# Kernel optimization log

Hardware: AMD Instinct MI355X
Metric: run time of the kernel (lower is better)

## Reference

```python
import jax, jax.numpy as jnp
import numpy as np

B, S, D_IN, D_OUT, H = 2, 2048, 1024, 1024, 16
HD = D_OUT // H


def setup_inputs() -> dict:
    key = jax.random.key(0)
    ks = jax.random.split(key, 7)
    sc = 0.02
    return {
        "x": jax.random.normal(ks[0], (B, S, D_IN), jnp.float32),
        "attention_mask": jnp.ones((B, S), dtype=bool),
        "W_query": jax.random.normal(ks[1], (D_IN, D_OUT), jnp.float32) * sc,
        "W_key": jax.random.normal(ks[2], (D_IN, D_OUT), jnp.float32) * sc,
        "W_value": jax.random.normal(ks[3], (D_IN, D_OUT), jnp.float32) * sc,
        "W_out": jax.random.normal(ks[4], (D_OUT, D_OUT), jnp.float32) * sc,
        "b_out": jnp.zeros((D_OUT,), jnp.float32),
    }


def reference(x, attention_mask, W_query, W_key, W_value, W_out, b_out):
    b, n, _ = x.shape
    # projections -> (b, H, n, hd)
    def split_heads(t):
        return t.reshape(b, n, H, HD).transpose(0, 2, 1, 3)
    q = split_heads(x @ W_query)
    k = split_heads(x @ W_key)
    v = split_heads(x @ W_value)
    scores = jnp.einsum("bhqd,bhkd->bhqk", q, k)  # (b,H,n,n)
    neg_inf = jnp.float32(-jnp.inf)
    causal = jnp.triu(jnp.ones((n, n), dtype=bool), k=1)  # True above diagonal
    scores = jnp.where(causal[None, None], neg_inf, scores)
    pad = attention_mask[:, None, None, :]  # (b,1,1,n)
    scores = jnp.where(~pad, neg_inf, scores)
    attn = jax.nn.softmax(scores / jnp.float32(np.sqrt(HD)), axis=-1)
    ctx = jnp.einsum("bhqk,bhkd->bhqd", attn, v)
    ctx = ctx.transpose(0, 2, 1, 3).reshape(b, n, D_OUT)
    return ctx @ W_out + b_out
```

## Files before the change

### kernel.cpp

```cpp
#include <hip/hip_runtime.h>
#include <hip/hip_bf16.h>

typedef __bf16 bf16;
typedef __bf16 bf16x4 __attribute__((ext_vector_type(4)));
typedef __bf16 bf16x8 __attribute__((ext_vector_type(8)));
typedef float  f32x4  __attribute__((ext_vector_type(4)));

#define B_    2
#define S_    2048
#define DIN   1024
#define DOUT  1024
#define H_    16
#define HD    64
#define M_TOT (B_ * S_)

__device__ __forceinline__ void gload16(const void* g, void* l) {
  __builtin_amdgcn_global_load_lds(
      (__attribute__((address_space(1))) void*)(g),
      (__attribute__((address_space(3))) void*)(l), 16, 0, 0);
}

__global__ __launch_bounds__(256) void cast_x_k(const float* __restrict__ x,
                                                bf16* __restrict__ xb, int n4) {
  int i = blockIdx.x * 256 + threadIdx.x;
  if (i < n4) {
    float4 v = ((const float4*)x)[i];
    bf16x4 o = {(bf16)v.x, (bf16)v.y, (bf16)v.z, (bf16)v.w};
    ((bf16x4*)xb)[i] = o;
  }
}

__global__ __launch_bounds__(256) void transpose_cast_k(
    const float* __restrict__ wq, const float* __restrict__ wk,
    const float* __restrict__ wv, const float* __restrict__ wo,
    bf16* __restrict__ wqkv_t, bf16* __restrict__ wot) {
  __shared__ float tile[32][33];
  const int z = blockIdx.z;
  const float* src = (z == 0) ? wq : (z == 1) ? wk : (z == 2) ? wv : wo;
  bf16* dst = (z < 3) ? (wqkv_t + (size_t)z * DOUT * DIN) : wot;
  const int bx = blockIdx.x * 32;
  const int by = blockIdx.y * 32;
  const int tx = threadIdx.x & 31, ty = threadIdx.x >> 5;
#pragma unroll
  for (int i = 0; i < 32; i += 8)
    tile[ty + i][tx] = src[(size_t)(by + ty + i) * DOUT + bx + tx];
  __syncthreads();
#pragma unroll
  for (int i = 0; i < 32; i += 8)
    dst[(size_t)(bx + ty + i) * DIN + by + tx] = (bf16)tile[tx][ty + i];
}

template <int MODE>
__global__ __launch_bounds__(256, 2) void gemm_k(
    const bf16* __restrict__ A, const bf16* __restrict__ Bt,
    bf16* __restrict__ Qb, bf16* __restrict__ Kb, bf16* __restrict__ Vt,
    float* __restrict__ Out, const float* __restrict__ bias, int N, int K) {
  __shared__ bf16 Als[128 * 64];
  __shared__ bf16 Bls[128 * 64];
  const int tid = threadIdx.x;
  const int m0 = blockIdx.x * 128, n0 = blockIdx.y * 128;
  const int lane = tid & 63, wave = tid >> 6;
  const int wr = wave >> 1, wc = wave & 1;
  f32x4 acc[4][4] = {};
  const int rowi = tid >> 3;
  const int coli = (tid & 7) * 8;

  for (int kt = 0; kt < K; kt += 64) {
#pragma unroll
    for (int j = 0; j < 4; ++j) {
      int r = j * 32 + rowi;
      gload16(A + (size_t)(m0 + r) * K + kt + coli, Als + r * 64 + coli);
      gload16(Bt + (size_t)(n0 + r) * K + kt + coli, Bls + r * 64 + coli);
    }
    asm volatile("s_waitcnt vmcnt(0)" ::: "memory");
    __syncthreads();
#pragma unroll
    for (int kk = 0; kk < 2; ++kk) {
      bf16x8 af[4], bfr[4];
      const int ko = kk * 32 + (lane >> 4) * 8;
#pragma unroll
      for (int mi = 0; mi < 4; ++mi)
        af[mi] = *(const bf16x8*)(Als + (wr * 64 + mi * 16 + (lane & 15)) * 64 + ko);
#pragma unroll
      for (int ni = 0; ni < 4; ++ni)
        bfr[ni] = *(const bf16x8*)(Bls + (wc * 64 + ni * 16 + (lane & 15)) * 64 + ko);
#pragma unroll
      for (int mi = 0; mi < 4; ++mi)
#pragma unroll
        for (int ni = 0; ni < 4; ++ni)
          acc[mi][ni] = __builtin_amdgcn_mfma_f32_16x16x32_bf16(
              af[mi], bfr[ni], acc[mi][ni], 0, 0, 0);
    }
    __syncthreads();
  }

#pragma unroll
  for (int mi = 0; mi < 4; ++mi) {
    const int gr0 = m0 + wr * 64 + mi * 16 + (lane >> 4) * 4;
#pragma unroll
    for (int ni = 0; ni < 4; ++ni) {
      const int gc = n0 + wc * 64 + ni * 16 + (lane & 15);
      if (MODE == 0) {
        const int mat = gc >> 10;
        const int c = gc & 1023;
        const int h = c >> 6, hd = c & 63;
        const int b = gr0 >> 11, s0 = gr0 & 2047;
        if (mat == 2) {
          bf16x4 pk;
#pragma unroll
          for (int r = 0; r < 4; ++r) pk[r] = (bf16)acc[mi][ni][r];
          *(bf16x4*)(Vt + ((size_t)((b * H_ + h) * HD + hd)) * S_ + s0) = pk;
        } else {
          bf16* dst = (mat == 0) ? Qb : Kb;
          const float sc = (mat == 0) ? 0.125f : 1.0f;
#pragma unroll
          for (int r = 0; r < 4; ++r)
            dst[((size_t)(b * H_ + h) * S_ + s0 + r) * HD + hd] =
                (bf16)(acc[mi][ni][r] * sc);
        }
      } else {
#pragma unroll
        for (int r = 0; r < 4; ++r)
          Out[(size_t)(gr0 + r) * N + gc] = acc[mi][ni][r] + bias[gc];
      }
    }
  }
}

__global__ __launch_bounds__(256, 1) void attn_k(
    const bf16* __restrict__ Qb, const bf16* __restrict__ Kb,
    const bf16* __restrict__ Vt, bf16* __restrict__ ctx) {
  __shared__ bf16 Kls[2][64 * 64];
  __shared__ bf16 Vls[2][64 * 64];
  __shared__ bf16 Pls[4][32 * 64];
  const int z = blockIdx.x;
  const int h = blockIdx.y, b = blockIdx.z;
  const int tid = threadIdx.x;
  const int lane = tid & 63, wave = tid >> 6;
  const int l15 = lane & 15, g = lane >> 4;
  const bf16* Qh = Qb + (size_t)(b * H_ + h) * S_ * HD;
  const bf16* Kh = Kb + (size_t)(b * H_ + h) * S_ * HD;
  const bf16* Vh = Vt + (size_t)(b * H_ + h) * HD * S_;

#define STAGE(tt, bb)                                                        \
  do {                                                                       \
    const int kv0s = (tt) * 64;                                              \
    _Pragma("unroll") for (int j = 0; j < 2; ++j) {                          \
      const int c = wave * 128 + j * 64 + lane;                              \
      const int row = c >> 3, cc = (c & 7) ^ (row & 7);                      \
      gload16(Kh + (size_t)(kv0s + row) * HD + cc * 8, &Kls[bb][c * 8]);     \
      gload16(Vh + (size_t)row * S_ + kv0s + cc * 8, &Vls[bb][c * 8]);       \
    }                                                                        \
  } while (0)

  for (int pi = 0; pi < 2; ++pi) {
    const int qt = pi ? (15 - z) : z;
    const int NT = 2 * qt + 2;
    const int q0w = qt * 128 + wave * 32;

    bf16x8 qa[2][2];
#pragma unroll
    for (int qf = 0; qf < 2; ++qf)
#pragma unroll
      for (int kk = 0; kk < 2; ++kk)
        qa[qf][kk] = *(const bf16x8*)(Qh + (size_t)(q0w + qf * 16 + l15) * HD +
                                      kk * 32 + g * 8);
    f32x4 o[2][4] = {};
    float m_run[2] = {-1e30f, -1e30f}, l_run[2] = {0.f, 0.f};

    STAGE(0, 0);
    asm volatile("s_waitcnt vmcnt(0)" ::: "memory");
    __builtin_amdgcn_s_barrier();

    for (int t = 0; t < NT; ++t) {
      const int cur = t & 1;
      if (t + 1 < NT) STAGE(t + 1, cur ^ 1);
      const int kv0 = t * 64;
      const bool dead = kv0 > q0w + 31;
      if (!dead) {
        f32x4 s[2][4] = {};
#pragma unroll
        for (int kk = 0; kk < 2; ++kk) {
          const int ko = kk * 32 + g * 8;
          bf16x8 kf[4];
#pragma unroll
          for (int ni = 0; ni < 4; ++ni) {
            const int r = ni * 16 + l15;
            kf[ni] = *(const bf16x8*)(&Kls[cur][(r * 64 + ko) ^ ((r & 7) << 3)]);
          }
#pragma unroll
          for (int qf = 0; qf < 2; ++qf)
#pragma unroll
            for (int ni = 0; ni < 4; ++ni)
              s[qf][ni] = __builtin_amdgcn_mfma_f32_16x16x32_bf16(
                  kf[ni], qa[qf][kk], s[qf][ni], 0, 0, 0);
        }
        if (kv0 + 63 > q0w) {
#pragma unroll
          for (int qf = 0; qf < 2; ++qf) {
            const int q = q0w + qf * 16 + l15;
#pragma unroll
            for (int ni = 0; ni < 4; ++ni) {
              const int kvb = kv0 + ni * 16 + g * 4;
#pragma unroll
              for (int r = 0; r < 4; ++r)
                if (kvb + r > q) s[qf][ni][r] = -1e30f;
            }
          }
        }
#pragma unroll
        for (int qf = 0; qf < 2; ++qf) {
          float mx = -1e30f;
#pragma unroll
          for (int ni = 0; ni < 4; ++ni)
#pragma unroll
            for (int r = 0; r < 4; ++r) mx = fmaxf(mx, s[qf][ni][r]);
          mx = fmaxf(mx, __shfl_xor(mx, 16, 64));
          mx = fmaxf(mx, __shfl_xor(mx, 32, 64));
          const float mnew = fmaxf(m_run[qf], mx);
          const float corr = __expf(m_run[qf] - mnew);
          m_run[qf] = mnew;
          float rs = 0.f;
          const int qloc = qf * 16 + l15;
#pragma unroll
          for (int ni = 0; ni < 4; ++ni) {
            bf16x4 pk;
#pragma unroll
            for (int r = 0; r < 4; ++r) {
              const float p = __expf(s[qf][ni][r] - mnew);
              rs += p;
              pk[r] = (bf16)p;
            }
            *(bf16x4*)(&Pls[wave][(qloc * 64 + ni * 16 + g * 4) ^
                                  ((qloc & 7) << 3)]) = pk;
          }
          rs += __shfl_xor(rs, 16, 64);
          rs += __shfl_xor(rs, 32, 64);
          l_run[qf] = l_run[qf] * corr + rs;
#pragma unroll
          for (int r = 0; r < 4; ++r) {
            const float cr = __shfl(corr, (lane & 48) | (g * 4 + r), 64);
#pragma unroll
            for (int ni = 0; ni < 4; ++ni) o[qf][ni][r] *= cr;
          }
        }
#pragma unroll
        for (int kk = 0; kk < 2; ++kk) {
          const int ko = kk * 32 + g * 8;
          bf16x8 vf[4];
#pragma unroll
          for (int ni = 0; ni < 4; ++ni) {
            const int r = ni * 16 + l15;
            vf[ni] = *(const bf16x8*)(&Vls[cur][(r * 64 + ko) ^ ((r & 7) << 3)]);
          }
#pragma unroll
          for (int qf = 0; qf < 2; ++qf) {
            const int qloc = qf * 16 + l15;
            const bf16x8 pa = *(const bf16x8*)(&Pls[wave][(qloc * 64 + ko) ^
                                                          ((qloc & 7) << 3)]);
#pragma unroll
            for (int ni = 0; ni < 4; ++ni)
              o[qf][ni] = __builtin_amdgcn_mfma_f32_16x16x32_bf16(
                  pa, vf[ni], o[qf][ni], 0, 0, 0);
          }
        }
      }
      if (t + 1 < NT) asm volatile("s_waitcnt vmcnt(0)" ::: "memory");
      __builtin_amdgcn_s_barrier();
    }

#pragma unroll
    for (int qf = 0; qf < 2; ++qf)
#pragma unroll
      for (int r = 0; r < 4; ++r) {
        const float ld = __shfl(l_run[qf], (lane & 48) | (g * 4 + r), 64);
        const float inv = 1.f / ld;
        const int row = b * S_ + qt * 128 + wave * 32 + qf * 16 + g * 4 + r;
#pragma unroll
        for (int ni = 0; ni < 4; ++ni)
          ctx[(size_t)row * DOUT + h * 64 + ni * 16 + l15] =
              (bf16)(o[qf][ni][r] * inv);
      }
  }
#undef STAGE
}

extern "C" void kernel_launch(void* const* d_in, const int* in_sizes, int n_in,
                              void* d_out, int out_size, void* d_ws, size_t ws_size,
                              hipStream_t stream) {
  const float* x  = (const float*)d_in[0];
  const float* wq = (const float*)d_in[2];
  const float* wk = (const float*)d_in[3];
  const float* wv = (const float*)d_in[4];
  const float* wo = (const float*)d_in[5];
  const float* bo = (const float*)d_in[6];
  float* out = (float*)d_out;

  char* p = (char*)d_ws;
  bf16* xb   = (bf16*)p; p += (size_t)M_TOT * DIN * 2;
  bf16* wqkv = (bf16*)p; p += (size_t)3 * DOUT * DIN * 2;
  bf16* wot  = (bf16*)p; p += (size_t)DOUT * DOUT * 2;
  bf16* Qb   = (bf16*)p; p += (size_t)B_ * H_ * S_ * HD * 2;
  bf16* Kb   = (bf16*)p; p += (size_t)B_ * H_ * S_ * HD * 2;
  bf16* Vt   = (bf16*)p; p += (size_t)B_ * H_ * S_ * HD * 2;
  bf16* ctx  = (bf16*)p; p += (size_t)M_TOT * DOUT * 2;

  cast_x_k<<<4096, 256, 0, stream>>>(x, xb, M_TOT * DIN / 4);
  transpose_cast_k<<<dim3(32, 32, 4), 256, 0, stream>>>(wq, wk, wv, wo, wqkv, wot);
  gemm_k<0><<<dim3(32, 24), 256, 0, stream>>>(xb, wqkv, Qb, Kb, Vt,
                                              nullptr, nullptr, 3 * DOUT, DIN);
  attn_k<<<dim3(8, H_, B_), 256, 0, stream>>>(Qb, Kb, Vt, ctx);
  gemm_k<1><<<dim3(32, 8), 256, 0, stream>>>(ctx, wot, nullptr, nullptr, nullptr,
                                             out, bo, DOUT, DOUT);
}
```

Before: 213.4 us.

## Shrink attention query tile to 64 rows and add lazy softmax rescaling

The attention kernel now gives each block 64 query rows (16 per wave) instead of 128. The grid doubles to 16x16x2 blocks, each still handling a pair of complementary causal tiles. Launch bounds now allow two blocks per CU. The online softmax skips the max update and output rescale unless some row's max grows by more than 8, which saves exp and shuffle work. In exchange, each loaded K/V tile is reused by fewer query rows, and the lagging max allows larger unnormalised exponents in the bf16 P values.

After: 197.0 us. 7.7% less time.

```diff
diff --git a/kernel.cpp b/kernel.cpp
--- a/kernel.cpp
+++ b/kernel.cpp
@@ -127,12 +127,12 @@
   }
 }
 
-__global__ __launch_bounds__(256, 1) void attn_k(
+__global__ __launch_bounds__(256, 2) void attn_k(
     const bf16* __restrict__ Qb, const bf16* __restrict__ Kb,
     const bf16* __restrict__ Vt, bf16* __restrict__ ctx) {
   __shared__ bf16 Kls[2][64 * 64];
   __shared__ bf16 Vls[2][64 * 64];
-  __shared__ bf16 Pls[4][32 * 64];
+  __shared__ bf16 Pls[4][16 * 64];
   const int z = blockIdx.x;
   const int h = blockIdx.y, b = blockIdx.z;
   const int tid = threadIdx.x;
@@ -154,19 +154,16 @@
   } while (0)
 
   for (int pi = 0; pi < 2; ++pi) {
-    const int qt = pi ? (15 - z) : z;
-    const int NT = 2 * qt + 2;
-    const int q0w = qt * 128 + wave * 32;
-
-    bf16x8 qa[2][2];
-#pragma unroll
-    for (int qf = 0; qf < 2; ++qf)
-#pragma unroll
-      for (int kk = 0; kk < 2; ++kk)
-        qa[qf][kk] = *(const bf16x8*)(Qh + (size_t)(q0w + qf * 16 + l15) * HD +
-                                      kk * 32 + g * 8);
-    f32x4 o[2][4] = {};
-    float m_run[2] = {-1e30f, -1e30f}, l_run[2] = {0.f, 0.f};
+    const int qt = pi ? (31 - z) : z;
+    const int NT = qt + 1;
+    const int q0w = qt * 64 + wave * 16;
+
+    bf16x8 qa[2];
+#pragma unroll
+    for (int kk = 0; kk < 2; ++kk)
+      qa[kk] = *(const bf16x8*)(Qh + (size_t)(q0w + l15) * HD + kk * 32 + g * 8);
+    f32x4 o[4] = {};
+    float m_run = -1e30f, l_run = 0.f;
 
     STAGE(0, 0);
     asm volatile("s_waitcnt vmcnt(0)" ::: "memory");
@@ -176,92 +173,76 @@
       const int cur = t & 1;
       if (t + 1 < NT) STAGE(t + 1, cur ^ 1);
       const int kv0 = t * 64;
-      const bool dead = kv0 > q0w + 31;
+      const bool dead = kv0 > q0w + 15;
       if (!dead) {
-        f32x4 s[2][4] = {};
+        f32x4 s[4] = {};
 #pragma unroll
         for (int kk = 0; kk < 2; ++kk) {
           const int ko = kk * 32 + g * 8;
-          bf16x8 kf[4];
 #pragma unroll
           for (int ni = 0; ni < 4; ++ni) {
             const int r = ni * 16 + l15;
-            kf[ni] = *(const bf16x8*)(&Kls[cur][(r * 64 + ko) ^ ((r & 7) << 3)]);
-          }
-#pragma unroll
-          for (int qf = 0; qf < 2; ++qf)
-#pragma unroll
-            for (int ni = 0; ni < 4; ++ni)
-              s[qf][ni] = __builtin_amdgcn_mfma_f32_16x16x32_bf16(
-                  kf[ni], qa[qf][kk], s[qf][ni], 0, 0, 0);
+            bf16x8 kf = *(const bf16x8*)(&Kls[cur][(r * 64 + ko) ^ ((r & 7) << 3)]);
+            s[ni] = __builtin_amdgcn_mfma_f32_16x16x32_bf16(
+                kf, qa[kk], s[ni], 0, 0, 0);
+          }
         }
         if (kv0 + 63 > q0w) {
-#pragma unroll
-          for (int qf = 0; qf < 2; ++qf) {
-            const int q = q0w + qf * 16 + l15;
-#pragma unroll
-            for (int ni = 0; ni < 4; ++ni) {
-              const int kvb = kv0 + ni * 16 + g * 4;
-#pragma unroll
-              for (int r = 0; r < 4; ++r)
-                if (kvb + r > q) s[qf][ni][r] = -1e30f;
-            }
-          }
-        }
-#pragma unroll
-        for (int qf = 0; qf < 2; ++qf) {
-          float mx = -1e30f;
-#pragma unroll
-          for (int ni = 0; ni < 4; ++ni)
-#pragma unroll
-            for (int r = 0; r < 4; ++r) mx = fmaxf(mx, s[qf][ni][r]);
-          mx = fmaxf(mx, __shfl_xor(mx, 16, 64));
-          mx = fmaxf(mx, __shfl_xor(mx, 32, 64));
-          const float mnew = fmaxf(m_run[qf], mx);
-          const float corr = __expf(m_run[qf] - mnew);
-          m_run[qf] = mnew;
-          float rs = 0.f;
-          const int qloc = qf * 16 + l15;
+          const int q = q0w + l15;
 #pragma unroll
           for (int ni = 0; ni < 4; ++ni) {
-            bf16x4 pk;
-#pragma unroll
-            for (int r = 0; r < 4; ++r) {
-              const float p = __expf(s[qf][ni][r] - mnew);
-              rs += p;
-              pk[r] = (bf16)p;
-            }
-            *(bf16x4*)(&Pls[wave][(qloc * 64 + ni * 16 + g * 4) ^
-                                  ((qloc & 7) << 3)]) = pk;
-          }
-          rs += __shfl_xor(rs, 16, 64);
-          rs += __shfl_xor(rs, 32, 64);
-          l_run[qf] = l_run[qf] * corr + rs;
+            const int kvb = kv0 + ni * 16 + g * 4;
+#pragma unroll
+            for (int r = 0; r < 4; ++r)
+              if (kvb + r > q) s[ni][r] = -1e30f;
+          }
+        }
+        float mx = -1e30f;
+#pragma unroll
+        for (int ni = 0; ni < 4; ++ni)
+#pragma unroll
+          for (int r = 0; r < 4; ++r) mx = fmaxf(mx, s[ni][r]);
+        mx = fmaxf(mx, __shfl_xor(mx, 16, 64));
+        mx = fmaxf(mx, __shfl_xor(mx, 32, 64));
+        if (!__all(mx - m_run <= 8.f)) {
+          const float mnew = fmaxf(m_run, mx);
+          const float corr = __expf(m_run - mnew);
+          m_run = mnew;
+          l_run *= corr;
 #pragma unroll
           for (int r = 0; r < 4; ++r) {
             const float cr = __shfl(corr, (lane & 48) | (g * 4 + r), 64);
 #pragma unroll
-            for (int ni = 0; ni < 4; ++ni) o[qf][ni][r] *= cr;
-          }
-        }
+            for (int ni = 0; ni < 4; ++ni) o[ni][r] *= cr;
+          }
+        }
+        float rs = 0.f;
+#pragma unroll
+        for (int ni = 0; ni < 4; ++ni) {
+          bf16x4 pk;
+#pragma unroll
+          for (int r = 0; r < 4; ++r) {
+            const float p = __expf(s[ni][r] - m_run);
+            rs += p;
+            pk[r] = (bf16)p;
+          }
+          *(bf16x4*)(&Pls[wave][(l15 * 64 + ni * 16 + g * 4) ^
+                                ((l15 & 7) << 3)]) = pk;
+        }
+        rs += __shfl_xor(rs, 16, 64);
+        rs += __shfl_xor(rs, 32, 64);
+        l_run += rs;
 #pragma unroll
         for (int kk = 0; kk < 2; ++kk) {
           const int ko = kk * 32 + g * 8;
-          bf16x8 vf[4];
+          const bf16x8 pa = *(const bf16x8*)(&Pls[wave][(l15 * 64 + ko) ^
+                                                        ((l15 & 7) << 3)]);
 #pragma unroll
           for (int ni = 0; ni < 4; ++ni) {
             const int r = ni * 16 + l15;
-            vf[ni] = *(const bf16x8*)(&Vls[cur][(r * 64 + ko) ^ ((r & 7) << 3)]);
-          }
-#pragma unroll
-          for (int qf = 0; qf < 2; ++qf) {
-            const int qloc = qf * 16 + l15;
-            const bf16x8 pa = *(const bf16x8*)(&Pls[wave][(qloc * 64 + ko) ^
-                                                          ((qloc & 7) << 3)]);
-#pragma unroll
-            for (int ni = 0; ni < 4; ++ni)
-              o[qf][ni] = __builtin_amdgcn_mfma_f32_16x16x32_bf16(
-                  pa, vf[ni], o[qf][ni], 0, 0, 0);
+            bf16x8 vf = *(const bf16x8*)(&Vls[cur][(r * 64 + ko) ^ ((r & 7) << 3)]);
+            o[ni] = __builtin_amdgcn_mfma_f32_16x16x32_bf16(
+                pa, vf, o[ni], 0, 0, 0);
           }
         }
       }
@@ -270,17 +251,15 @@
     }
 
 #pragma unroll
-    for (int qf = 0; qf < 2; ++qf)
-#pragma unroll
-      for (int r = 0; r < 4; ++r) {
-        const float ld = __shfl(l_run[qf], (lane & 48) | (g * 4 + r), 64);
-        const float inv = 1.f / ld;
-        const int row = b * S_ + qt * 128 + wave * 32 + qf * 16 + g * 4 + r;
-#pragma unroll
-        for (int ni = 0; ni < 4; ++ni)
-          ctx[(size_t)row * DOUT + h * 64 + ni * 16 + l15] =
-              (bf16)(o[qf][ni][r] * inv);
-      }
+    for (int r = 0; r < 4; ++r) {
+      const float ld = __shfl(l_run, (lane & 48) | (g * 4 + r), 64);
+      const float inv = 1.f / ld;
+      const int row = b * S_ + q0w + g * 4 + r;
+#pragma unroll
+      for (int ni = 0; ni < 4; ++ni)
+        ctx[(size_t)row * DOUT + h * 64 + ni * 16 + l15] =
+            (bf16)(o[ni][r] * inv);
+    }
   }
 #undef STAGE
 }
@@ -309,7 +288,7 @@
   transpose_cast_k<<<dim3(32, 32, 4), 256, 0, stream>>>(wq, wk, wv, wo, wqkv, wot);
   gemm_k<0><<<dim3(32, 24), 256, 0, stream>>>(xb, wqkv, Qb, Kb, Vt,
                                               nullptr, nullptr, 3 * DOUT, DIN);
-  attn_k<<<dim3(8, H_, B_), 256, 0, stream>>>(Qb, Kb, Vt, ctx);
+  attn_k<<<dim3(16, H_, B_), 256, 0, stream>>>(Qb, Kb, Vt, ctx);
   gemm_k<1><<<dim3(32, 8), 256, 0, stream>>>(ctx, wot, nullptr, nullptr, nullptr,
                                              out, bo, DOUT, DOUT);
 }
```
